# Performance work log

Hardware: AMD Instinct MI355X
Metric: run time of the kernel (lower is better)

## Reference

```python
import jax, jax.numpy as jnp
import numpy as np

NUM_HEAD = 8
HEAD_DIM = 64
MAX_LEN = 2048
FEAT_DIM = 512
BATCH = 2
TEMPERATURE = 10000.0


def positional_encoding(L, F, temperature=TEMPERATURE):
    # Faithful port of get_positional_encoding (torch.range is inclusive -> L / F elements)
    embed = jnp.arange(L, dtype=jnp.float32)
    dim_t = jnp.arange(F, dtype=jnp.float32)
    dim_t = temperature ** (2.0 * jnp.floor(dim_t / 2.0) / F)
    pos = embed[:, None] / dim_t                      # (L, F)
    pos = jnp.stack([jnp.sin(pos[:, 0::2]), jnp.cos(pos[:, 1::2])], axis=2)  # (L, F//2, 2)
    return pos.reshape(1, L, F)


def setup_inputs() -> dict:
    key = jax.random.key(0)
    ks = jax.random.split(key, 7)
    D = NUM_HEAD * HEAD_DIM
    scale = 1.0 / np.sqrt(FEAT_DIM)
    return {
        "inputs": jax.random.normal(ks[0], (BATCH, FEAT_DIM, MAX_LEN), dtype=jnp.float32),
        "Wq": jax.random.normal(ks[1], (D, FEAT_DIM), dtype=jnp.float32) * scale,
        "bq": jax.random.normal(ks[2], (D,), dtype=jnp.float32) * 0.01,
        "Wk": jax.random.normal(ks[3], (D, FEAT_DIM), dtype=jnp.float32) * scale,
        "bk": jax.random.normal(ks[4], (D,), dtype=jnp.float32) * 0.01,
        "Wv": jax.random.normal(ks[5], (D, FEAT_DIM), dtype=jnp.float32) * scale,
        "bv": jax.random.normal(ks[6], (D,), dtype=jnp.float32) * 0.01,
    }


def reference(inputs, Wq, bq, Wk, bk, Wv, bv):
    B, F, L = inputs.shape
    H, d = NUM_HEAD, HEAD_DIM
    pos = positional_encoding(L, F)                   # (1, L, F)
    x = jnp.transpose(inputs, (0, 2, 1))              # (B, L, F)
    qk_in = x + pos
    q = (qk_in @ Wq.T + bq).reshape(B, L, H, d)       # (B, L, H, d)
    k = (qk_in @ Wk.T + bk).reshape(B, L, H, d)
    v = x @ Wv.T + bv                                 # computed but unused (bug in original)
    del v
    # NOTE: original uses KEY heads as values (multi_head_value built from key)
    scores = jnp.einsum("bqhd,bkhd->bhqk", q, k) * (float(d) ** -0.5)
    attn = jax.nn.softmax(scores, axis=-1)            # (B, H, L, L)
    dist = jnp.einsum("bhqk,bkhd->bqhd", attn, k).reshape(B, L, H * d)
    attn_out = jnp.transpose(attn, (0, 2, 3, 1))      # (B, L, L, H) == cat of head splits on -1
    return dist, attn_out
```

## Files before the change

kernel.cpp:

```cpp
#include <hip/hip_runtime.h>
#include <math.h>

constexpr int LSEQ = 2048;
constexpr int FEAT = 512;
constexpr int NH = 8;
constexpr int DM = 512;
constexpr int NB = 2;

typedef __bf16 bf16x8 __attribute__((ext_vector_type(8)));
typedef unsigned short u16x8 __attribute__((ext_vector_type(8)));
typedef unsigned int u32x4 __attribute__((ext_vector_type(4)));
typedef float f32x4 __attribute__((ext_vector_type(4)));

__device__ inline f32x4 mfma16(u16x8 a, u16x8 b, f32x4 c) {
  return __builtin_amdgcn_mfma_f32_16x16x32_bf16(
      __builtin_bit_cast(bf16x8, a), __builtin_bit_cast(bf16x8, b), c, 0, 0, 0);
}
__device__ inline unsigned cvtpk(float lo, float hi) {
  unsigned r;
  asm("v_cvt_pk_bf16_f32 %0, %1, %2" : "=v"(r) : "v"(lo), "v"(hi));
  return r;
}
__device__ inline u16x8 ldbf8(const unsigned short* p) {
  return *reinterpret_cast<const u16x8*>(p);
}

__global__ __launch_bounds__(256) void pos_kernel(float* __restrict__ posT) {
  int idx = blockIdx.x * 256 + threadIdx.x;
  int l = idx & (LSEQ - 1);
  int f = idx >> 11;
  int i = f >> 1;
  double t = exp((double)i * (9.210340371976184 / 256.0));
  float ang = (float)((double)l / t);
  posT[idx] = (f & 1) ? cosf(ang) : sinf(ang);
}

__global__ __launch_bounds__(256) void prep_kernel(const float* __restrict__ x,
                                                   const float* __restrict__ posT,
                                                   unsigned short* __restrict__ abuf) {
  __shared__ float As[64 * 68];
  const int t = threadIdx.x;
  const int bid = blockIdx.x;
  const int ft = bid & 7, lt = (bid >> 3) & 31, b = bid >> 8;
  const int f0 = ft * 64, l0 = lt * 64;
#pragma unroll
  for (int rep = 0; rep < 4; ++rep) {
    int fl = rep * 16 + (t >> 4), l4 = (t & 15) * 4;
    float4 xv = *(const float4*)(x + ((size_t)b * FEAT + f0 + fl) * LSEQ + l0 + l4);
    float4 pv = *(const float4*)(posT + (size_t)(f0 + fl) * LSEQ + l0 + l4);
    *(float4*)&As[fl * 68 + l4] = make_float4(xv.x + pv.x, xv.y + pv.y, xv.z + pv.z, xv.w + pv.w);
  }
  __syncthreads();
  const int ll = t >> 2, fc = t & 3;
#pragma unroll
  for (int rep = 0; rep < 4; ++rep) {
    int fb = (fc + rep * 4) * 4;
    float v0 = As[(fb + 0) * 68 + ll];
    float v1 = As[(fb + 1) * 68 + ll];
    float v2 = As[(fb + 2) * 68 + ll];
    float v3 = As[(fb + 3) * 68 + ll];
    uint2 u = make_uint2(cvtpk(v0, v1), cvtpk(v2, v3));
    *(uint2*)(abuf + ((size_t)(b * LSEQ + l0 + ll)) * 512 + f0 + fb) = u;
  }
}

__global__ __launch_bounds__(256) void wcvt_kernel(const float* __restrict__ Wq,
                                                   const float* __restrict__ Wk,
                                                   unsigned short* __restrict__ wbuf) {
  int i8 = blockIdx.x * 256 + threadIdx.x;
  size_t base = (size_t)i8 * 8;
  const float* src = (base < (size_t)512 * 512) ? Wq + base : Wk + (base - (size_t)512 * 512);
  float4 a = *(const float4*)src;
  float4 b4 = *(const float4*)(src + 4);
  *(uint2*)(wbuf + base) = make_uint2(cvtpk(a.x, a.y), cvtpk(a.z, a.w));
  *(uint2*)(wbuf + base + 4) = make_uint2(cvtpk(b4.x, b4.y), cvtpk(b4.z, b4.w));
}

__global__ __launch_bounds__(256) void proj_kernel(
    const unsigned short* __restrict__ abuf, const unsigned short* __restrict__ wbuf,
    const float* __restrict__ bq, const float* __restrict__ bk,
    unsigned short* __restrict__ qb, unsigned short* __restrict__ kb,
    unsigned short* __restrict__ kT) {
  const int t = threadIdx.x;
  const int c0 = blockIdx.x * 64;
  const int r0 = blockIdx.y * 64;
  const int w = t >> 6, l = t & 63;
  const int lr = l & 15, g = l >> 4;
  const int c0w = c0 + (w >> 1) * 32;
  const int r0w = r0 + (w & 1) * 32;
  f32x4 acc[2][2];
#pragma unroll
  for (int i = 0; i < 2; ++i)
#pragma unroll
    for (int j = 0; j < 2; ++j) acc[i][j] = (f32x4){0.f, 0.f, 0.f, 0.f};
  for (int f0 = 0; f0 < FEAT; f0 += 32) {
    u16x8 a0 = ldbf8(wbuf + (size_t)(c0w + lr) * 512 + f0 + g * 8);
    u16x8 a1 = ldbf8(wbuf + (size_t)(c0w + 16 + lr) * 512 + f0 + g * 8);
    u16x8 b0 = ldbf8(abuf + (size_t)(r0w + lr) * 512 + f0 + g * 8);
    u16x8 b1 = ldbf8(abuf + (size_t)(r0w + 16 + lr) * 512 + f0 + g * 8);
    acc[0][0] = mfma16(a0, b0, acc[0][0]);
    acc[0][1] = mfma16(a0, b1, acc[0][1]);
    acc[1][0] = mfma16(a1, b0, acc[1][0]);
    acc[1][1] = mfma16(a1, b1, acc[1][1]);
  }
  const int isK = (c0 >= DM);
  const float* bias = isK ? bk : bq;
  unsigned short* ob = isK ? kb : qb;
  const int cb = c0w & (DM - 1);
#pragma unroll
  for (int ch = 0; ch < 2; ++ch) {
    int c = cb + ch * 16 + g * 4;
    float b0v = bias[c], b1v = bias[c + 1], b2v = bias[c + 2], b3v = bias[c + 3];
#pragma unroll
    for (int rh = 0; rh < 2; ++rh) {
      int r = r0w + rh * 16 + lr;
      f32x4 v = acc[ch][rh];
      uint2 u = make_uint2(cvtpk(v[0] + b0v, v[1] + b1v), cvtpk(v[2] + b2v, v[3] + b3v));
      *(uint2*)(ob + (size_t)r * 512 + c) = u;
      if (isK) {
        int bsel = r >> 11, lq = r & (LSEQ - 1);
        unsigned short* kp = kT + ((size_t)(bsel * 512 + c)) * 2048 + lq;
        kp[0] = (unsigned short)(u.x & 0xffff);
        kp[2048] = (unsigned short)(u.x >> 16);
        kp[2 * 2048] = (unsigned short)(u.y & 0xffff);
        kp[3 * 2048] = (unsigned short)(u.y >> 16);
      }
    }
  }
}

__global__ __launch_bounds__(512) void pass1_kernel(
    const unsigned short* __restrict__ qb, const unsigned short* __restrict__ kb,
    float* __restrict__ lpart) {
  const int t = threadIdx.x;
  const int bid = blockIdx.x;
  const int sp = bid & 3, qt = (bid >> 2) & 63, b = bid >> 8;
  const int q0 = qt * 32;
  const int h = t >> 6, l = t & 63;
  const int lr = l & 15, g = l >> 4;
  u16x8 qf[2][2];
#pragma unroll
  for (int Mt = 0; Mt < 2; ++Mt)
#pragma unroll
    for (int dh = 0; dh < 2; ++dh)
      qf[Mt][dh] = ldbf8(qb + (size_t)(b * LSEQ + q0 + Mt * 16 + lr) * 512 + h * 64 + dh * 32 + g * 8);
  float sum[2] = {0.f, 0.f};
  for (int slab = 0; slab < 16; ++slab) {
    const int kk0 = sp * 512 + slab * 32;
    u16x8 af[2][2];
#pragma unroll
    for (int kh = 0; kh < 2; ++kh)
#pragma unroll
      for (int dh = 0; dh < 2; ++dh)
        af[kh][dh] = ldbf8(kb + (size_t)(b * LSEQ + kk0 + kh * 16 + lr) * 512 + h * 64 + dh * 32 + g * 8);
#pragma unroll
    for (int Mt = 0; Mt < 2; ++Mt)
#pragma unroll
      for (int kh = 0; kh < 2; ++kh) {
        f32x4 s = (f32x4){0.f, 0.f, 0.f, 0.f};
        s = mfma16(af[kh][0], qf[Mt][0], s);
        s = mfma16(af[kh][1], qf[Mt][1], s);
        sum[Mt] += __expf(s[0] * 0.125f) + __expf(s[1] * 0.125f) +
                   __expf(s[2] * 0.125f) + __expf(s[3] * 0.125f);
      }
  }
#pragma unroll
  for (int Mt = 0; Mt < 2; ++Mt) {
    float v = sum[Mt];
    v += __shfl_xor(v, 16);
    v += __shfl_xor(v, 32);
    if ((l & 48) == 0)
      lpart[((size_t)((b * 4 + sp) * LSEQ) + q0 + Mt * 16 + lr) * 8 + h] = v;
  }
}

__global__ __launch_bounds__(512) void pass2_kernel(
    const unsigned short* __restrict__ qb, const unsigned short* __restrict__ kb,
    const unsigned short* __restrict__ kT, const float* __restrict__ lpart,
    float* __restrict__ attn, float* __restrict__ distp, int log2S) {
  __shared__ float Ps[32 * 292];
  __shared__ float linv[256];
  const int t = threadIdx.x;
  const int bid = blockIdx.x;
  const int S = 1 << log2S;
  const int sp = bid & (S - 1);
  const int qt = (bid >> log2S) & 63;
  const int b = bid >> (6 + log2S);
  const int q0 = qt * 32;
  if (t < 256) {
    int q = t >> 3, hh = t & 7;
    float s = 0.f;
#pragma unroll
    for (int p = 0; p < 4; ++p)
      s += lpart[((size_t)((b * 4 + p) * LSEQ) + q0 + q) * 8 + hh];
    linv[t] = 1.0f / s;
  }
  __syncthreads();
  const int h = t >> 6, l = t & 63;
  const int lr = l & 15, g = l >> 4;
  u16x8 qf[2][2];
#pragma unroll
  for (int Mt = 0; Mt < 2; ++Mt)
#pragma unroll
    for (int dh = 0; dh < 2; ++dh)
      qf[Mt][dh] = ldbf8(qb + (size_t)(b * LSEQ + q0 + Mt * 16 + lr) * 512 + h * 64 + dh * 32 + g * 8);
  float lv[2] = {linv[lr * 8 + h], linv[(16 + lr) * 8 + h]};
  f32x4 dacc[2][4];
#pragma unroll
  for (int Mt = 0; Mt < 2; ++Mt)
#pragma unroll
    for (int Nd = 0; Nd < 4; ++Nd) dacc[Mt][Nd] = (f32x4){0.f, 0.f, 0.f, 0.f};

  const int nslab = 64 >> log2S;
  const int kkb = sp * (2048 >> log2S);
  for (int slab = 0; slab < nslab; ++slab) {
    const int kk0 = kkb + slab * 32;
    u16x8 af[2][2];
#pragma unroll
    for (int kh = 0; kh < 2; ++kh)
#pragma unroll
      for (int dh = 0; dh < 2; ++dh)
        af[kh][dh] = ldbf8(kb + (size_t)(b * LSEQ + kk0 + kh * 16 + lr) * 512 + h * 64 + dh * 32 + g * 8);
    u16x8 bt[4];
#pragma unroll
    for (int Nd = 0; Nd < 4; ++Nd)
      bt[Nd] = ldbf8(kT + (size_t)(b * 512 + h * 64 + Nd * 16 + lr) * 2048 + kk0 + g * 8);
#pragma unroll
    for (int Mt = 0; Mt < 2; ++Mt)
#pragma unroll
      for (int kh = 0; kh < 2; ++kh) {
        f32x4 s = (f32x4){0.f, 0.f, 0.f, 0.f};
        s = mfma16(af[kh][0], qf[Mt][0], s);
        s = mfma16(af[kh][1], qf[Mt][1], s);
        float e0 = __expf(s[0] * 0.125f) * lv[Mt];
        float e1 = __expf(s[1] * 0.125f) * lv[Mt];
        float e2 = __expf(s[2] * 0.125f) * lv[Mt];
        float e3 = __expf(s[3] * 0.125f) * lv[Mt];
        int base = (Mt * 16 + lr) * 292 + h * 36 + kh * 16 + g * 4;
        *(float2*)&Ps[base] = make_float2(e0, e1);
        *(float2*)&Ps[base + 2] = make_float2(e2, e3);
      }
    __syncthreads();
#pragma unroll
    for (int rep = 0; rep < 4; ++rep) {
      int F = rep * 512 + t;
      int q = F >> 6, kk = (F >> 1) & 31, hh = (F & 1) * 4;
      int pb = q * 292 + hh * 36 + kk;
      float4 v = make_float4(Ps[pb], Ps[pb + 36], Ps[pb + 72], Ps[pb + 108]);
      *(float4*)(attn + ((size_t)(b * LSEQ + q0 + q)) * (LSEQ * NH) + (size_t)(kk0 + kk) * 8 + hh) = v;
    }
#pragma unroll
    for (int Mt = 0; Mt < 2; ++Mt) {
      int pb = (Mt * 16 + lr) * 292 + h * 36 + g * 8;
      f32x4 plo = *(const f32x4*)&Ps[pb];
      f32x4 phi = *(const f32x4*)&Ps[pb + 4];
      u32x4 pu = {cvtpk(plo[0], plo[1]), cvtpk(plo[2], plo[3]),
                  cvtpk(phi[0], phi[1]), cvtpk(phi[2], phi[3])};
      u16x8 pa = __builtin_bit_cast(u16x8, pu);
#pragma unroll
      for (int Nd = 0; Nd < 4; ++Nd)
        dacc[Mt][Nd] = mfma16(pa, bt[Nd], dacc[Mt][Nd]);
    }
    __syncthreads();
  }
  float* dp = distp + (size_t)sp * (NB * LSEQ * DM);
#pragma unroll
  for (int Mt = 0; Mt < 2; ++Mt)
#pragma unroll
    for (int Nd = 0; Nd < 4; ++Nd)
#pragma unroll
      for (int r = 0; r < 4; ++r)
        dp[((size_t)(b * LSEQ + q0 + Mt * 16 + g * 4 + r)) * 512 + h * 64 + Nd * 16 + lr] =
            dacc[Mt][Nd][r];
}

__global__ __launch_bounds__(256) void combine_kernel(const float* __restrict__ p,
                                                      float* __restrict__ dist) {
  int i4 = blockIdx.x * 256 + threadIdx.x;
  const int N4 = (NB * LSEQ * DM) / 4;
  const float4* p4 = (const float4*)p;
  float4 a = p4[i4], c = p4[N4 + i4];
  ((float4*)dist)[i4] = make_float4(a.x + c.x, a.y + c.y, a.z + c.z, a.w + c.w);
}

extern "C" void kernel_launch(void* const* d_in, const int* in_sizes, int n_in,
                              void* d_out, int out_size, void* d_ws, size_t ws_size,
                              hipStream_t stream) {
  const float* x  = (const float*)d_in[0];
  const float* Wq = (const float*)d_in[1];
  const float* bq = (const float*)d_in[2];
  const float* Wk = (const float*)d_in[3];
  const float* bk = (const float*)d_in[4];
  float* out  = (float*)d_out;
  float* dist = out;
  float* attn = out + (size_t)NB * LSEQ * DM;
  float* ws = (float*)d_ws;
  float* posT  = ws;
  float* lpart = ws + 1048576;
  unsigned short* abuf = (unsigned short*)(ws + 1179648);
  unsigned short* wbuf = (unsigned short*)(ws + 2228224);
  unsigned short* qb   = (unsigned short*)(ws + 2490368);
  unsigned short* kb   = (unsigned short*)(ws + 3538944);
  unsigned short* kT   = (unsigned short*)(ws + 4587520);
  float* distp = ws + 5636096;
  const int log2S = (ws_size >= (size_t)(5636096 + 2ull * 2097152) * 4) ? 1 : 0;

  pos_kernel<<<4096, 256, 0, stream>>>(posT);
  prep_kernel<<<512, 256, 0, stream>>>(x, posT, abuf);
  wcvt_kernel<<<256, 256, 0, stream>>>(Wq, Wk, wbuf);
  proj_kernel<<<dim3(16, 64), 256, 0, stream>>>(abuf, wbuf, bq, bk, qb, kb, kT);
  pass1_kernel<<<512, 512, 0, stream>>>(qb, kb, lpart);
  float* dtarget = (log2S == 0) ? dist : distp;
  pass2_kernel<<<NB * 64 * (1 << log2S), 512, 0, stream>>>(qb, kb, kT, lpart, attn, dtarget, log2S);
  if (log2S)
    combine_kernel<<<2048, 256, 0, stream>>>(distp, dist);
}
```

Baseline: 178.9 us.

## Double-buffer softmax tile, split pass2 keys in two, retile pass1, use exp2

Pass2 now always splits the key range across two blocks. Its shared P tile is double-buffered, which removes the second barrier per slab, and the large attn output is written with nontemporal stores. Pass1 is retiled to 64 queries by 8 key splits, and exp is computed as exp2 with a folded scale constant. The workspace is repacked so one split's partial dist reuses the pos buffer and the other writes dist directly, which a simplified combine kernel then sums. This trades a guaranteed combine pass and more LDS per block for fewer barriers and less cache pollution from the attn write.

```diff
diff --git a/kernel.cpp b/kernel.cpp
--- a/kernel.cpp
+++ b/kernel.cpp
@@ -11,6 +11,8 @@
 typedef unsigned short u16x8 __attribute__((ext_vector_type(8)));
 typedef unsigned int u32x4 __attribute__((ext_vector_type(4)));
 typedef float f32x4 __attribute__((ext_vector_type(4)));
+
+#define EXPC 0.18033688011112042f
 
 __device__ inline f32x4 mfma16(u16x8 a, u16x8 b, f32x4 c) {
   return __builtin_amdgcn_mfma_f32_16x16x32_bf16(
@@ -134,19 +136,19 @@
     float* __restrict__ lpart) {
   const int t = threadIdx.x;
   const int bid = blockIdx.x;
-  const int sp = bid & 3, qt = (bid >> 2) & 63, b = bid >> 8;
-  const int q0 = qt * 32;
+  const int sp = bid & 7, qt = (bid >> 3) & 31, b = bid >> 8;
+  const int q0 = qt * 64;
   const int h = t >> 6, l = t & 63;
   const int lr = l & 15, g = l >> 4;
-  u16x8 qf[2][2];
-#pragma unroll
-  for (int Mt = 0; Mt < 2; ++Mt)
+  u16x8 qf[4][2];
+#pragma unroll
+  for (int Mt = 0; Mt < 4; ++Mt)
 #pragma unroll
     for (int dh = 0; dh < 2; ++dh)
       qf[Mt][dh] = ldbf8(qb + (size_t)(b * LSEQ + q0 + Mt * 16 + lr) * 512 + h * 64 + dh * 32 + g * 8);
-  float sum[2] = {0.f, 0.f};
-  for (int slab = 0; slab < 16; ++slab) {
-    const int kk0 = sp * 512 + slab * 32;
+  float sum[4] = {0.f, 0.f, 0.f, 0.f};
+  for (int slab = 0; slab < 8; ++slab) {
+    const int kk0 = sp * 256 + slab * 32;
     u16x8 af[2][2];
 #pragma unroll
     for (int kh = 0; kh < 2; ++kh)
@@ -154,45 +156,44 @@
       for (int dh = 0; dh < 2; ++dh)
         af[kh][dh] = ldbf8(kb + (size_t)(b * LSEQ + kk0 + kh * 16 + lr) * 512 + h * 64 + dh * 32 + g * 8);
 #pragma unroll
-    for (int Mt = 0; Mt < 2; ++Mt)
+    for (int Mt = 0; Mt < 4; ++Mt)
 #pragma unroll
       for (int kh = 0; kh < 2; ++kh) {
         f32x4 s = (f32x4){0.f, 0.f, 0.f, 0.f};
         s = mfma16(af[kh][0], qf[Mt][0], s);
         s = mfma16(af[kh][1], qf[Mt][1], s);
-        sum[Mt] += __expf(s[0] * 0.125f) + __expf(s[1] * 0.125f) +
-                   __expf(s[2] * 0.125f) + __expf(s[3] * 0.125f);
+        sum[Mt] += exp2f(s[0] * EXPC) + exp2f(s[1] * EXPC) +
+                   exp2f(s[2] * EXPC) + exp2f(s[3] * EXPC);
       }
   }
 #pragma unroll
-  for (int Mt = 0; Mt < 2; ++Mt) {
+  for (int Mt = 0; Mt < 4; ++Mt) {
     float v = sum[Mt];
     v += __shfl_xor(v, 16);
     v += __shfl_xor(v, 32);
     if ((l & 48) == 0)
-      lpart[((size_t)((b * 4 + sp) * LSEQ) + q0 + Mt * 16 + lr) * 8 + h] = v;
+      lpart[((size_t)((b * 8 + sp) * LSEQ) + q0 + Mt * 16 + lr) * 8 + h] = v;
   }
 }
 
 __global__ __launch_bounds__(512) void pass2_kernel(
     const unsigned short* __restrict__ qb, const unsigned short* __restrict__ kb,
     const unsigned short* __restrict__ kT, const float* __restrict__ lpart,
-    float* __restrict__ attn, float* __restrict__ distp, int log2S) {
-  __shared__ float Ps[32 * 292];
+    float* __restrict__ attn, float* __restrict__ dist, float* __restrict__ distp) {
+  __shared__ float Ps[2 * 32 * 292];
   __shared__ float linv[256];
   const int t = threadIdx.x;
   const int bid = blockIdx.x;
-  const int S = 1 << log2S;
-  const int sp = bid & (S - 1);
-  const int qt = (bid >> log2S) & 63;
-  const int b = bid >> (6 + log2S);
+  const int qt = bid & 63;
+  const int sp = (bid >> 6) & 1;
+  const int b = bid >> 7;
   const int q0 = qt * 32;
   if (t < 256) {
     int q = t >> 3, hh = t & 7;
     float s = 0.f;
 #pragma unroll
-    for (int p = 0; p < 4; ++p)
-      s += lpart[((size_t)((b * 4 + p) * LSEQ) + q0 + q) * 8 + hh];
+    for (int p = 0; p < 8; ++p)
+      s += lpart[((size_t)((b * 8 + p) * LSEQ) + q0 + q) * 8 + hh];
     linv[t] = 1.0f / s;
   }
   __syncthreads();
@@ -211,10 +212,10 @@
 #pragma unroll
     for (int Nd = 0; Nd < 4; ++Nd) dacc[Mt][Nd] = (f32x4){0.f, 0.f, 0.f, 0.f};
 
-  const int nslab = 64 >> log2S;
-  const int kkb = sp * (2048 >> log2S);
-  for (int slab = 0; slab < nslab; ++slab) {
+  const int kkb = sp * 1024;
+  for (int slab = 0; slab < 32; ++slab) {
     const int kk0 = kkb + slab * 32;
+    float* Pc = &Ps[(slab & 1) * 9344];
     u16x8 af[2][2];
 #pragma unroll
     for (int kh = 0; kh < 2; ++kh)
@@ -232,13 +233,9 @@
         f32x4 s = (f32x4){0.f, 0.f, 0.f, 0.f};
         s = mfma16(af[kh][0], qf[Mt][0], s);
         s = mfma16(af[kh][1], qf[Mt][1], s);
-        float e0 = __expf(s[0] * 0.125f) * lv[Mt];
-        float e1 = __expf(s[1] * 0.125f) * lv[Mt];
-        float e2 = __expf(s[2] * 0.125f) * lv[Mt];
-        float e3 = __expf(s[3] * 0.125f) * lv[Mt];
-        int base = (Mt * 16 + lr) * 292 + h * 36 + kh * 16 + g * 4;
-        *(float2*)&Ps[base] = make_float2(e0, e1);
-        *(float2*)&Ps[base + 2] = make_float2(e2, e3);
+        f32x4 e = {exp2f(s[0] * EXPC) * lv[Mt], exp2f(s[1] * EXPC) * lv[Mt],
+                   exp2f(s[2] * EXPC) * lv[Mt], exp2f(s[3] * EXPC) * lv[Mt]};
+        *(f32x4*)&Pc[(Mt * 16 + lr) * 292 + h * 36 + kh * 16 + g * 4] = e;
       }
     __syncthreads();
 #pragma unroll
@@ -246,14 +243,15 @@
       int F = rep * 512 + t;
       int q = F >> 6, kk = (F >> 1) & 31, hh = (F & 1) * 4;
       int pb = q * 292 + hh * 36 + kk;
-      float4 v = make_float4(Ps[pb], Ps[pb + 36], Ps[pb + 72], Ps[pb + 108]);
-      *(float4*)(attn + ((size_t)(b * LSEQ + q0 + q)) * (LSEQ * NH) + (size_t)(kk0 + kk) * 8 + hh) = v;
+      f32x4 v = {Pc[pb], Pc[pb + 36], Pc[pb + 72], Pc[pb + 108]};
+      __builtin_nontemporal_store(v,
+          (f32x4*)(attn + ((size_t)(b * LSEQ + q0 + q)) * (LSEQ * NH) + (size_t)(kk0 + kk) * 8 + hh));
     }
 #pragma unroll
     for (int Mt = 0; Mt < 2; ++Mt) {
       int pb = (Mt * 16 + lr) * 292 + h * 36 + g * 8;
-      f32x4 plo = *(const f32x4*)&Ps[pb];
-      f32x4 phi = *(const f32x4*)&Ps[pb + 4];
+      f32x4 plo = *(const f32x4*)&Pc[pb];
+      f32x4 phi = *(const f32x4*)&Pc[pb + 4];
       u32x4 pu = {cvtpk(plo[0], plo[1]), cvtpk(plo[2], plo[3]),
                   cvtpk(phi[0], phi[1]), cvtpk(phi[2], phi[3])};
       u16x8 pa = __builtin_bit_cast(u16x8, pu);
@@ -261,9 +259,8 @@
       for (int Nd = 0; Nd < 4; ++Nd)
         dacc[Mt][Nd] = mfma16(pa, bt[Nd], dacc[Mt][Nd]);
     }
-    __syncthreads();
-  }
-  float* dp = distp + (size_t)sp * (NB * LSEQ * DM);
+  }
+  float* dp = sp ? distp : dist;
 #pragma unroll
   for (int Mt = 0; Mt < 2; ++Mt)
 #pragma unroll
@@ -277,9 +274,8 @@
 __global__ __launch_bounds__(256) void combine_kernel(const float* __restrict__ p,
                                                       float* __restrict__ dist) {
   int i4 = blockIdx.x * 256 + threadIdx.x;
-  const int N4 = (NB * LSEQ * DM) / 4;
   const float4* p4 = (const float4*)p;
-  float4 a = p4[i4], c = p4[N4 + i4];
+  float4 a = ((float4*)dist)[i4], c = p4[i4];
   ((float4*)dist)[i4] = make_float4(a.x + c.x, a.y + c.y, a.z + c.z, a.w + c.w);
 }
 
@@ -296,22 +292,19 @@
   float* attn = out + (size_t)NB * LSEQ * DM;
   float* ws = (float*)d_ws;
   float* posT  = ws;
-  float* lpart = ws + 1048576;
-  unsigned short* abuf = (unsigned short*)(ws + 1179648);
-  unsigned short* wbuf = (unsigned short*)(ws + 2228224);
-  unsigned short* qb   = (unsigned short*)(ws + 2490368);
-  unsigned short* kb   = (unsigned short*)(ws + 3538944);
-  unsigned short* kT   = (unsigned short*)(ws + 4587520);
-  float* distp = ws + 5636096;
-  const int log2S = (ws_size >= (size_t)(5636096 + 2ull * 2097152) * 4) ? 1 : 0;
+  unsigned short* abuf = (unsigned short*)(ws + 1048576);
+  unsigned short* wbuf = (unsigned short*)(ws + 2097152);
+  unsigned short* qb   = (unsigned short*)(ws + 2359296);
+  unsigned short* kb   = (unsigned short*)(ws + 3407872);
+  unsigned short* kT   = (unsigned short*)(ws + 4456448);
+  float* lpart = ws + 5505024;
+  float* distp = ws;
 
   pos_kernel<<<4096, 256, 0, stream>>>(posT);
   prep_kernel<<<512, 256, 0, stream>>>(x, posT, abuf);
   wcvt_kernel<<<256, 256, 0, stream>>>(Wq, Wk, wbuf);
   proj_kernel<<<dim3(16, 64), 256, 0, stream>>>(abuf, wbuf, bq, bk, qb, kb, kT);
   pass1_kernel<<<512, 512, 0, stream>>>(qb, kb, lpart);
-  float* dtarget = (log2S == 0) ? dist : distp;
-  pass2_kernel<<<NB * 64 * (1 << log2S), 512, 0, stream>>>(qb, kb, kT, lpart, attn, dtarget, log2S);
-  if (log2S)
-    combine_kernel<<<2048, 256, 0, stream>>>(distp, dist);
-}
+  pass2_kernel<<<256, 512, 0, stream>>>(qb, kb, kT, lpart, attn, dist, distp);
+  combine_kernel<<<2048, 256, 0, stream>>>(distp, dist);
+}
```

New measurement: 171.1 us. 4.4% less time.
